# Performance work log

Hardware: AMD Instinct MI355X
Metric: run time of the kernel (lower is better)

The kernel has to match this reference:

```python
import jax, jax.numpy as jnp
import numpy as np


def setup_inputs() -> dict:
    key0 = jax.random.key(0)
    kq, kk, kv = jax.random.split(key0, 3)
    B, S, E = 4, 2048, 1024
    query = jax.random.normal(kq, (B, S, E), dtype=jnp.float32)
    key = jax.random.normal(kk, (B, S, E), dtype=jnp.float32)
    value = jax.random.normal(kv, (B, S, E), dtype=jnp.float32)
    attn_mask = jnp.zeros((B, S, S), dtype=jnp.float32)
    return {"query": query, "key": key, "value": value, "attn_mask": attn_mask}


def reference(query, key, value, attn_mask):
    # qk = Q K^T / sqrt(E) + mask; softmax over last dim; dropout is
    # identity in eval mode (reference baseline); out = attn @ V.
    E = query.shape[-1]
    scale = 1.0 / jnp.sqrt(jnp.asarray(E, dtype=query.dtype))
    qk = jnp.einsum("bqe,bke->bqk", query, key) * scale + attn_mask
    attn = jax.nn.softmax(qk, axis=-1)
    out = jnp.einsum("bqk,bke->bqe", attn, value)
    return out
```

## Files before the change

### kernel.cpp

```cpp
#include <hip/hip_runtime.h>
#include <stdint.h>
#include <math.h>

typedef unsigned short u16;
typedef short bf16x8 __attribute__((ext_vector_type(8)));
typedef unsigned short u16x8 __attribute__((ext_vector_type(8)));
typedef unsigned short u16x4 __attribute__((ext_vector_type(4)));
typedef float f32x4 __attribute__((ext_vector_type(4)));

#define LOG2E 1.4426950408889634f

__device__ __forceinline__ float bf2f(u16 u) {
  union { unsigned int i; float f; } v; v.i = ((unsigned int)u) << 16; return v.f;
}
__device__ __forceinline__ u16 f2bf(float f) {
  union { float ff; unsigned int i; } v; v.ff = f;
  unsigned int x = v.i;
  return (u16)((x + 0x7FFFu + ((x >> 16) & 1u)) >> 16);
}

__global__ __launch_bounds__(256)
void cvt_f32_bf16(const float* __restrict__ src, u16* __restrict__ dst, long n)
{
  long i = ((long)blockIdx.x * 256 + threadIdx.x) * 8;
  if (i + 8 > n) return;
  f32x4 a = *(const f32x4*)&src[i];
  f32x4 b = *(const f32x4*)&src[i + 4];
  u16x8 o;
#pragma unroll
  for (int j = 0; j < 4; j++) { o[j] = f2bf(a[j]); o[4 + j] = f2bf(b[j]); }
  *(u16x8*)&dst[i] = o;
}

__global__ __launch_bounds__(256)
void transcvt_v(const float* __restrict__ V, u16* __restrict__ VT, int S, int E)
{
  __shared__ u16 t[64][72];
  const int b = blockIdx.z;
  const float* Vb = V + (long)b * S * E;
  u16* VTb = VT + (long)b * S * E;
  const int k0 = blockIdx.x * 64, n0 = blockIdx.y * 64;
  const int tid = threadIdx.x;
#pragma unroll
  for (int p = 0; p < 2; p++) {
    int kk = p * 32 + (tid >> 3);
    int nn = (tid & 7) * 8;
    f32x4 a = *(const f32x4*)&Vb[(long)(k0 + kk) * E + n0 + nn];
    f32x4 c = *(const f32x4*)&Vb[(long)(k0 + kk) * E + n0 + nn + 4];
#pragma unroll
    for (int j = 0; j < 4; j++) { t[nn + j][kk] = f2bf(a[j]); t[nn + 4 + j][kk] = f2bf(c[j]); }
  }
  __syncthreads();
#pragma unroll
  for (int p = 0; p < 2; p++) {
    int nn = p * 32 + (tid >> 3);
    int kk = (tid & 7) * 8;
    u16x8 u;
#pragma unroll
    for (int j = 0; j < 8; j++) u[j] = t[nn][kk + j];
    *(u16x8*)&VTb[(long)(n0 + nn) * S + k0 + kk] = u;
  }
}

template<int ASRC, int BSRC, int BMODE, int HASMASK, int COUT>
__global__ __launch_bounds__(256, 2)
void gemm_bt(const void* __restrict__ Ap, int lda, long aRowOff,
             const void* __restrict__ Bp, int ldb, long bBatchStride,
             void* __restrict__ Cp, int ldc, long cRowOff,
             const float* __restrict__ maskf,
             int K, float scale, long g0, int S)
{
  const int tid  = threadIdx.x;
  const int lane = tid & 63;
  const int wave = tid >> 6;
  const long gTile = g0 + (long)blockIdx.y * 128;
  const int  b     = (int)(gTile / S);
  const int  nTile = blockIdx.x * 128;

  __shared__ u16 As[128][40];
  __shared__ u16 Bs[128][40];

  const int qm = (wave >> 1) * 64;
  const int qn = (wave & 1) * 64;

  f32x4 acc[4][4];
#pragma unroll
  for (int i = 0; i < 4; i++)
#pragma unroll
    for (int j = 0; j < 4; j++) acc[i][j] = (f32x4){0.f, 0.f, 0.f, 0.f};

  const u16*   Ab = (const u16*)Ap   + (gTile - aRowOff) * (long)lda;
  const float* Af = (const float*)Ap + (gTile - aRowOff) * (long)lda;
  const u16*   Bb = (const u16*)Bp   + (long)b * bBatchStride;
  const float* Bf = (const float*)Bp + (long)b * bBatchStride;

  const int lm = lane & 15;
  const int lk = (lane >> 4) * 8;

  for (int k0 = 0; k0 < K; k0 += 32) {
    if (ASRC == 0) {
      int srow = tid >> 2, scol = (tid & 3) * 8;
#pragma unroll
      for (int p = 0; p < 2; p++) {
        int r = p * 64 + srow;
        *(u16x8*)&As[r][scol] = *(const u16x8*)&Ab[(long)r * lda + k0 + scol];
      }
    } else {
      int srow = tid >> 3, scol = (tid & 7) * 4;
#pragma unroll
      for (int p = 0; p < 4; p++) {
        int r = p * 32 + srow;
        f32x4 a = *(const f32x4*)&Af[(long)r * lda + k0 + scol];
        u16x4 o;
#pragma unroll
        for (int j = 0; j < 4; j++) o[j] = f2bf(a[j]);
        *(u16x4*)&As[r][scol] = o;
      }
    }
    if (BMODE == 0) {
      if (BSRC == 0) {
        int srow = tid >> 2, scol = (tid & 3) * 8;
#pragma unroll
        for (int p = 0; p < 2; p++) {
          int r = p * 64 + srow;
          *(u16x8*)&Bs[r][scol] = *(const u16x8*)&Bb[(long)(nTile + r) * ldb + k0 + scol];
        }
      } else {
        int srow = tid >> 3, scol = (tid & 7) * 4;
#pragma unroll
        for (int p = 0; p < 4; p++) {
          int r = p * 32 + srow;
          f32x4 a = *(const f32x4*)&Bf[(long)(nTile + r) * ldb + k0 + scol];
          u16x4 o;
#pragma unroll
          for (int j = 0; j < 4; j++) o[j] = f2bf(a[j]);
          *(u16x4*)&Bs[r][scol] = o;
        }
      }
    }
    __syncthreads();

    bf16x8 af[4], bfr[4];
#pragma unroll
    for (int rt = 0; rt < 4; rt++)
      af[rt] = *(const bf16x8*)&As[qm + rt * 16 + lm][lk];
    if (BMODE == 0) {
#pragma unroll
      for (int ct = 0; ct < 4; ct++)
        bfr[ct] = *(const bf16x8*)&Bs[qn + ct * 16 + lm][lk];
    } else {
#pragma unroll
      for (int ct = 0; ct < 4; ct++) {
        const float* vp = Bf + (long)(k0 + lk) * ldb + nTile + qn + ct * 16 + lm;
#pragma unroll
        for (int j = 0; j < 8; j++) bfr[ct][j] = (short)f2bf(vp[(long)j * ldb]);
      }
    }
#pragma unroll
    for (int rt = 0; rt < 4; rt++)
#pragma unroll
      for (int ct = 0; ct < 4; ct++)
        acc[rt][ct] = __builtin_amdgcn_mfma_f32_16x16x32_bf16(af[rt], bfr[ct], acc[rt][ct], 0, 0, 0);
    __syncthreads();
  }

  const int lr = (lane >> 4) * 4;
#pragma unroll
  for (int rt = 0; rt < 4; rt++) {
#pragma unroll
    for (int ct = 0; ct < 4; ct++) {
      long gr = gTile + qm + rt * 16 + lr;
      int  cc = nTile + qn + ct * 16 + lm;
#pragma unroll
      for (int i = 0; i < 4; i++) {
        float v = acc[rt][ct][i] * scale;
        if (HASMASK) v += maskf[(gr + i) * (long)ldc + cc];
        if (COUT == 0)
          ((u16*)Cp)[(gr + i - cRowOff) * (long)ldc + cc] = f2bf(v);
        else
          ((float*)Cp)[(gr + i - cRowOff) * (long)ldc + cc] = v;
      }
    }
  }
}

__global__ __launch_bounds__(256)
void softmax_rows(u16* __restrict__ Sbuf, int ncols)
{
  const long row = blockIdx.x;
  u16* rp = Sbuf + row * (long)ncols;
  const int tid = threadIdx.x;

  u16x8 u = *(const u16x8*)&rp[tid * 8];
  float x[8];
  float m = -3.0e38f;
#pragma unroll
  for (int i = 0; i < 8; i++) { x[i] = bf2f(u[i]); m = fmaxf(m, x[i]); }
#pragma unroll
  for (int off = 32; off; off >>= 1) m = fmaxf(m, __shfl_xor(m, off, 64));
  __shared__ float redm[4];
  if ((tid & 63) == 0) redm[tid >> 6] = m;
  __syncthreads();
  m = fmaxf(fmaxf(redm[0], redm[1]), fmaxf(redm[2], redm[3]));

  float e[8];
  float s = 0.f;
#pragma unroll
  for (int i = 0; i < 8; i++) { e[i] = exp2f((x[i] - m) * LOG2E); s += e[i]; }
#pragma unroll
  for (int off = 32; off; off >>= 1) s += __shfl_xor(s, off, 64);
  __shared__ float reds[4];
  if ((tid & 63) == 0) reds[tid >> 6] = s;
  __syncthreads();
  s = reds[0] + reds[1] + reds[2] + reds[3];

  float inv = 1.0f / s;
  u16x8 o;
#pragma unroll
  for (int i = 0; i < 8; i++) o[i] = f2bf(e[i] * inv);
  *(u16x8*)&rp[tid * 8] = o;
}

extern "C" void kernel_launch(void* const* d_in, const int* in_sizes, int n_in,
                              void* d_out, int out_size, void* d_ws, size_t ws_size,
                              hipStream_t stream)
{
  const float* Q    = (const float*)d_in[0];
  const float* Km   = (const float*)d_in[1];
  const float* V    = (const float*)d_in[2];
  const float* mask = (const float*)d_in[3];
  float* out = (float*)d_out;

  const long qsz = in_sizes[0];
  const long msz = in_sizes[3];
  const long E = 1024;
  const long S = (msz / qsz) * E;
  const long B = qsz / (S * E);
  const long G = B * S;
  const float scale = 1.0f / sqrtf((float)E);

  const size_t convBytes = (size_t)(3 * qsz) * 2;
  const size_t rowBytes  = (size_t)S * 2;
  char* w = (char*)d_ws;
  size_t avail = ws_size;
  const bool haveConv = (ws_size >= convBytes + 128 * rowBytes);

  u16 *Qb = nullptr, *Kb = nullptr, *VTb = nullptr;
  if (haveConv) {
    Qb  = (u16*)w;              w += (size_t)qsz * 2;
    Kb  = (u16*)w;              w += (size_t)qsz * 2;
    VTb = (u16*)w;              w += (size_t)qsz * 2;
    avail -= convBytes;
  }
  long Rmax = (long)((avail / rowBytes) / 128) * 128;
  if (Rmax > G) Rmax = G;
  if (Rmax < 128) Rmax = 128;
  u16* Sbuf = (u16*)w;

  if (haveConv) {
    cvt_f32_bf16<<<dim3((unsigned)(qsz / 2048)), 256, 0, stream>>>(Q, Qb, qsz);
    cvt_f32_bf16<<<dim3((unsigned)(qsz / 2048)), 256, 0, stream>>>(Km, Kb, qsz);
    transcvt_v<<<dim3(S / 64, E / 64, B), 256, 0, stream>>>(V, VTb, (int)S, (int)E);
  }

  for (long g0 = 0; g0 < G; g0 += Rmax) {
    const long R = (G - g0 < Rmax) ? (G - g0) : Rmax;
    if (haveConv) {
      gemm_bt<0, 0, 0, 1, 0><<<dim3(S / 128, R / 128), 256, 0, stream>>>(
          Qb, (int)E, 0L, Kb, (int)E, S * E,
          Sbuf, (int)S, g0, mask, (int)E, scale, g0, (int)S);
    } else {
      gemm_bt<1, 1, 0, 1, 0><<<dim3(S / 128, R / 128), 256, 0, stream>>>(
          Q, (int)E, 0L, Km, (int)E, S * E,
          Sbuf, (int)S, g0, mask, (int)E, scale, g0, (int)S);
    }
    softmax_rows<<<dim3(R), 256, 0, stream>>>(Sbuf, (int)S);
    if (haveConv) {
      gemm_bt<0, 0, 0, 0, 1><<<dim3(E / 128, R / 128), 256, 0, stream>>>(
          Sbuf, (int)S, g0, VTb, (int)S, E * S,
          out, (int)E, 0L, nullptr, (int)S, 1.0f, g0, (int)S);
    } else {
      gemm_bt<0, 1, 1, 0, 1><<<dim3(E / 128, R / 128), 256, 0, stream>>>(
          Sbuf, (int)S, g0, V, (int)E, S * E,
          out, (int)E, 0L, nullptr, (int)S, 1.0f, g0, (int)S);
    }
  }
}
```

Before: 303.6 us.

## Add bf16 GEMM using direct global-to-LDS loads and XCD-aware block remapping

Introduces a new bf16 GEMM kernel for the converted-input path. It loads tiles straight from global memory into LDS with global_load_lds, bypassing registers, and remaps block IDs so consecutive tiles land on the same XCD for better L2 reuse. It also raises the occupancy hint to 3 blocks per CU. The main loop is single-buffered with two barriers per K-step, so load latency may stay exposed. The LDS layout has no padding, so fragment reads may hit bank conflicts.

Result: faster. 288.9 us (-4.9%).

```diff
diff --git a/kernel.cpp b/kernel.cpp
--- a/kernel.cpp
+++ b/kernel.cpp
@@ -7,6 +7,9 @@
 typedef unsigned short u16x8 __attribute__((ext_vector_type(8)));
 typedef unsigned short u16x4 __attribute__((ext_vector_type(4)));
 typedef float f32x4 __attribute__((ext_vector_type(4)));
+
+typedef __attribute__((address_space(1))) const void gvoid;
+typedef __attribute__((address_space(3))) void lvoid;
 
 #define LOG2E 1.4426950408889634f
 
@@ -59,6 +62,102 @@
 #pragma unroll
     for (int j = 0; j < 8; j++) u[j] = t[nn][kk + j];
     *(u16x8*)&VTb[(long)(n0 + nn) * S + k0 + kk] = u;
+  }
+}
+
+template<int HASMASK, int COUT>
+__global__ __launch_bounds__(256, 3)
+void gemm_bt_fast(const u16* __restrict__ A, int lda, long aRowOff,
+                  const u16* __restrict__ B, int ldb, long bBatchStride,
+                  void* __restrict__ Cp, int ldc, long cRowOff,
+                  const float* __restrict__ maskf,
+                  int K, float scale, long g0, int S, int nbx)
+{
+  const int tid  = threadIdx.x;
+  const int lane = tid & 63;
+  const int wave = tid >> 6;
+
+  const int nwg  = gridDim.x;
+  const int orig = blockIdx.x;
+  const int q = nwg >> 3, r = nwg & 7;
+  const int xcd = orig & 7, slot = orig >> 3;
+  const int wgid = (xcd < r ? xcd * (q + 1) : r * (q + 1) + (xcd - r) * q) + slot;
+  const int by = wgid / nbx;
+  const int bx = wgid - by * nbx;
+
+  const long gTile = g0 + (long)by * 128;
+  const int  bidx  = (int)(gTile / S);
+  const int  nTile = bx * 128;
+
+  __shared__ u16 As[128][32];
+  __shared__ u16 Bs[128][32];
+
+  const u16* Ab = A + (gTile - aRowOff) * (long)lda;
+  const u16* Bb = B + (long)bidx * bBatchStride + (long)nTile * ldb;
+
+  const int qm = (wave >> 1) * 64;
+  const int qn = (wave & 1) * 64;
+  const int lm  = lane & 15;
+  const int lkB = (lane >> 4) * 16;
+
+  const int sr = lane >> 2;
+  const int sc = (lane & 3) * 8;
+
+  f32x4 acc[4][4];
+#pragma unroll
+  for (int i = 0; i < 4; i++)
+#pragma unroll
+    for (int j = 0; j < 4; j++) acc[i][j] = (f32x4){0.f, 0.f, 0.f, 0.f};
+
+  for (int k0 = 0; k0 < K; k0 += 32) {
+#pragma unroll
+    for (int p = 0; p < 2; p++) {
+      const int chunk = wave * 2 + p;
+      const int rr = chunk * 16 + sr;
+      __builtin_amdgcn_global_load_lds(
+          (gvoid*)&Ab[(long)rr * lda + k0 + sc],
+          (lvoid*)((char*)&As[0][0] + chunk * 1024),
+          16, 0, 0);
+      __builtin_amdgcn_global_load_lds(
+          (gvoid*)&Bb[(long)rr * ldb + k0 + sc],
+          (lvoid*)((char*)&Bs[0][0] + chunk * 1024),
+          16, 0, 0);
+    }
+    __syncthreads();
+
+    bf16x8 af[4], bfr[4];
+#pragma unroll
+    for (int rt = 0; rt < 4; rt++)
+      af[rt] = *(const bf16x8*)((const char*)&As[qm + rt * 16 + lm][0] + lkB);
+#pragma unroll
+    for (int ct = 0; ct < 4; ct++)
+      bfr[ct] = *(const bf16x8*)((const char*)&Bs[qn + ct * 16 + lm][0] + lkB);
+
+#pragma unroll
+    for (int rt = 0; rt < 4; rt++)
+#pragma unroll
+      for (int ct = 0; ct < 4; ct++)
+        acc[rt][ct] = __builtin_amdgcn_mfma_f32_16x16x32_bf16(af[rt], bfr[ct], acc[rt][ct], 0, 0, 0);
+    __syncthreads();
+  }
+
+  const int lr = (lane >> 4) * 4;
+#pragma unroll
+  for (int rt = 0; rt < 4; rt++) {
+#pragma unroll
+    for (int ct = 0; ct < 4; ct++) {
+      long gr = gTile + qm + rt * 16 + lr;
+      int  cc = nTile + qn + ct * 16 + lm;
+#pragma unroll
+      for (int i = 0; i < 4; i++) {
+        float v = acc[rt][ct][i] * scale;
+        if (HASMASK) v += maskf[(gr + i) * (long)ldc + cc];
+        if (COUT == 0)
+          ((u16*)Cp)[(gr + i - cRowOff) * (long)ldc + cc] = f2bf(v);
+        else
+          ((float*)Cp)[(gr + i - cRowOff) * (long)ldc + cc] = v;
+      }
+    }
   }
 }
 
@@ -266,9 +365,10 @@
   for (long g0 = 0; g0 < G; g0 += Rmax) {
     const long R = (G - g0 < Rmax) ? (G - g0) : Rmax;
     if (haveConv) {
-      gemm_bt<0, 0, 0, 1, 0><<<dim3(S / 128, R / 128), 256, 0, stream>>>(
+      const int nbx1 = (int)(S / 128);
+      gemm_bt_fast<1, 0><<<dim3((unsigned)(nbx1 * (R / 128))), 256, 0, stream>>>(
           Qb, (int)E, 0L, Kb, (int)E, S * E,
-          Sbuf, (int)S, g0, mask, (int)E, scale, g0, (int)S);
+          Sbuf, (int)S, g0, mask, (int)E, scale, g0, (int)S, nbx1);
     } else {
       gemm_bt<1, 1, 0, 1, 0><<<dim3(S / 128, R / 128), 256, 0, stream>>>(
           Q, (int)E, 0L, Km, (int)E, S * E,
@@ -276,9 +376,10 @@
     }
     softmax_rows<<<dim3(R), 256, 0, stream>>>(Sbuf, (int)S);
     if (haveConv) {
-      gemm_bt<0, 0, 0, 0, 1><<<dim3(E / 128, R / 128), 256, 0, stream>>>(
+      const int nbx2 = (int)(E / 128);
+      gemm_bt_fast<0, 1><<<dim3((unsigned)(nbx2 * (R / 128))), 256, 0, stream>>>(
           Sbuf, (int)S, g0, VTb, (int)S, E * S,
-          out, (int)E, 0L, nullptr, (int)S, 1.0f, g0, (int)S);
+          out, (int)E, 0L, nullptr, (int)S, 1.0f, g0, (int)S, nbx2);
     } else {
       gemm_bt<0, 1, 1, 0, 1><<<dim3(E / 128, R / 128), 256, 0, stream>>>(
           Sbuf, (int)S, g0, V, (int)E, S * E,
```
